# Performance work log

Hardware: AMD Instinct MI355X
Metric: run time of the kernel (lower is better)

The kernel has to match this reference:

```python
import jax, jax.numpy as jnp
import numpy as np

EPS = 1e-5
N_NODES = 100000
C_IN = 128
C_OUT = 128
N_EDGES = 3200000


def setup_inputs() -> dict:
    key = jax.random.key(0)
    k1, k2, k3 = jax.random.split(key, 3)
    x = jax.random.normal(k1, (N_NODES, C_IN), dtype=jnp.float32)
    edge_index = jax.random.randint(k2, (2, N_EDGES), 0, N_NODES, dtype=jnp.int64)
    # BatchNorm1d affine params
    gamma = jnp.ones((C_IN,), dtype=jnp.float32)
    beta = jnp.zeros((C_IN,), dtype=jnp.float32)
    # GCNConv linear weight (glorot) and bias
    limit = np.sqrt(6.0 / (C_IN + C_OUT)).astype(np.float32)
    W = jax.random.uniform(k3, (C_IN, C_OUT), minval=-limit, maxval=limit, dtype=jnp.float32)
    b = jnp.zeros((C_OUT,), dtype=jnp.float32)
    return {"x": x, "edge_index": edge_index, "gamma": gamma, "beta": beta, "W": W, "b": b}


def reference(x, edge_index, gamma, beta, W, b):
    n = x.shape[0]
    # --- BatchNorm1d (training mode: batch statistics, biased variance) ---
    mean = jnp.mean(x, axis=0)
    var = jnp.mean(jnp.square(x - mean), axis=0)
    xn = (x - mean) * jax.lax.rsqrt(var + EPS) * gamma + beta
    # --- GCNConv: linear, add self-loops, symmetric normalization, scatter-add ---
    h = xn @ W  # [n, C_out]
    loops = jnp.arange(n, dtype=edge_index.dtype)
    row = jnp.concatenate([edge_index[0], loops])  # source nodes
    col = jnp.concatenate([edge_index[1], loops])  # target nodes
    deg = jax.ops.segment_sum(jnp.ones_like(col, dtype=h.dtype), col, num_segments=n)
    dis = jnp.where(deg > 0, jax.lax.rsqrt(jnp.maximum(deg, 1.0)), 0.0)
    norm = dis[row] * dis[col]  # [E+n]
    msg = h[row] * norm[:, None]  # gather + scale
    out = jax.ops.segment_sum(msg, col, num_segments=n) + b  # scatter-add
    return jax.nn.relu(out)
```

## Files before the change

kernel.cpp:

```cpp
#include <hip/hip_runtime.h>

#define EPS_BN 1e-5f
#define C 128
#define CG 32
#define CAP 6144
#define NBLK 256

typedef __attribute__((ext_vector_type(8))) short bf16x8;
typedef __attribute__((ext_vector_type(4))) float f32x4;

__device__ inline unsigned bf16_rne(float f) {
  unsigned u = __float_as_uint(f);
  return (u + 0x7FFFu + ((u >> 16) & 1u)) >> 16;
}
__device__ inline float bf16_f(unsigned h) { return __uint_as_float(h << 16); }

__global__ void k_init(float* __restrict__ sums) {
  int i = blockIdx.x * blockDim.x + threadIdx.x;
  if (i < 256) sums[i] = 0.0f;
}

__global__ void k_stats(const float4* __restrict__ x4, float* __restrict__ sums, int n) {
  __shared__ float4 s_s[256];
  __shared__ float4 s_q[256];
  int t = threadIdx.x;
  int cg = t & 31;
  int rl = t >> 5;
  float4 s = make_float4(0.f, 0.f, 0.f, 0.f);
  float4 q = make_float4(0.f, 0.f, 0.f, 0.f);
  for (int r = blockIdx.x * 8 + rl; r < n; r += gridDim.x * 8) {
    float4 v = x4[(size_t)r * CG + cg];
    s.x += v.x; s.y += v.y; s.z += v.z; s.w += v.w;
    q.x += v.x * v.x; q.y += v.y * v.y; q.z += v.z * v.z; q.w += v.w * v.w;
  }
  s_s[t] = s; s_q[t] = q;
  __syncthreads();
  if (t < 32) {
    for (int j = 1; j < 8; ++j) {
      float4 a = s_s[t + 32 * j];
      float4 b = s_q[t + 32 * j];
      s.x += a.x; s.y += a.y; s.z += a.z; s.w += a.w;
      q.x += b.x; q.y += b.y; q.z += b.z; q.w += b.w;
    }
    atomicAdd(&sums[t * 4 + 0], s.x);
    atomicAdd(&sums[t * 4 + 1], s.y);
    atomicAdd(&sums[t * 4 + 2], s.z);
    atomicAdd(&sums[t * 4 + 3], s.w);
    atomicAdd(&sums[C + t * 4 + 0], q.x);
    atomicAdd(&sums[C + t * 4 + 1], q.y);
    atomicAdd(&sums[C + t * 4 + 2], q.z);
    atomicAdd(&sums[C + t * 4 + 3], q.w);
  }
}

__global__ void k_finalize(const float* __restrict__ sums,
                           const float* __restrict__ gamma,
                           const float* __restrict__ beta,
                           float* __restrict__ scale, float* __restrict__ shift,
                           int n) {
  int c = threadIdx.x;
  if (c < C) {
    float inv_n = 1.0f / (float)n;
    float mean = sums[c] * inv_n;
    float var = sums[C + c] * inv_n - mean * mean;
    float rstd = rsqrtf(var + EPS_BN);
    float sc = gamma[c] * rstd;
    scale[c] = sc;
    shift[c] = beta[c] - mean * sc;
  }
}

__global__ void k_hist(const int* __restrict__ col, int* __restrict__ histG,
                       int E, int NB, int chunk) {
  __shared__ int h[800];
  int b = blockIdx.x, t = threadIdx.x;
  for (int i = t; i < NB; i += 256) h[i] = 0;
  __syncthreads();
  int s = b * chunk, eend = min(E, s + chunk);
  for (int e = s + t; e < eend; e += 256) atomicAdd(&h[col[e] >> 7], 1);
  __syncthreads();
  for (int i = t; i < NB; i += 256) histG[b * NB + i] = h[i];
}

__global__ void k_scanH(int* __restrict__ histG, int* __restrict__ btot, int NB) {
  __shared__ int sh[NBLK];
  int q = blockIdx.x, t = threadIdx.x;
  int v = histG[t * NB + q];
  sh[t] = v;
  __syncthreads();
  for (int off = 1; off < NBLK; off <<= 1) {
    int a = (t >= off) ? sh[t - off] : 0;
    __syncthreads();
    sh[t] += a;
    __syncthreads();
  }
  histG[t * NB + q] = sh[t] - v;
  if (t == NBLK - 1) btot[q] = sh[t];
}

__global__ void k_scanB(const int* __restrict__ btot, int* __restrict__ boffs,
                        int NB, int E) {
  __shared__ int sh[1024];
  int t = threadIdx.x;
  int v = (t < NB) ? btot[t] : 0;
  sh[t] = v;
  __syncthreads();
  for (int off = 1; off < 1024; off <<= 1) {
    int a = (t >= off) ? sh[t - off] : 0;
    __syncthreads();
    sh[t] += a;
    __syncthreads();
  }
  if (t < NB) boffs[t] = sh[t] - v;
  if (t == 0) boffs[NB] = E;
}

__global__ void k_part(const int* __restrict__ row, const int* __restrict__ col,
                       const int* __restrict__ histG, const int* __restrict__ boffs,
                       unsigned* __restrict__ binned, int E, int NB, int chunk) {
  __shared__ int cur[800];
  int b = blockIdx.x, t = threadIdx.x;
  for (int i = t; i < NB; i += 256) cur[i] = boffs[i] + histG[b * NB + i];
  __syncthreads();
  int s = b * chunk, eend = min(E, s + chunk);
  for (int e = s + t; e < eend; e += 256) {
    int c = col[e];
    int pos = atomicAdd(&cur[c >> 7], 1);
    binned[pos] = ((unsigned)(c & 127) << 17) | (unsigned)row[e];
  }
}

__global__ __launch_bounds__(256) void k_reorder(
    unsigned* __restrict__ binned, const int* __restrict__ boffs,
    int* __restrict__ noffs, float* __restrict__ dis, int n, int E) {
  __shared__ int cnt[128];
  __shared__ int offs[128];
  __shared__ int cur[128];
  __shared__ int scn[128];
  __shared__ unsigned list[CAP];
  int b = blockIdx.x, t = threadIdx.x;
  if (t < 128) cnt[t] = 0;
  __syncthreads();
  int s = boffs[b], e = boffs[b + 1];
  for (int i = s + t; i < e; i += 256) atomicAdd(&cnt[binned[i] >> 17], 1);
  __syncthreads();
  if (t < 128) scn[t] = cnt[t];
  __syncthreads();
  for (int off = 1; off < 128; off <<= 1) {
    int a = (t >= off && t < 128) ? scn[t - off] : 0;
    __syncthreads();
    if (t < 128) scn[t] += a;
    __syncthreads();
  }
  if (t < 128) {
    offs[t] = scn[t] - cnt[t];
    cur[t] = scn[t] - cnt[t];
  }
  __syncthreads();
  for (int i = s + t; i < e; i += 256) {
    unsigned v = binned[i];
    int pos = atomicAdd(&cur[v >> 17], 1);
    if (pos < CAP) list[pos] = v & 0x1FFFFu;
  }
  __syncthreads();
  int len = e - s;
  for (int i = t; i < len; i += 256) binned[s + i] = list[i];
  int node = b * 128 + t;
  if (t < 128 && node < n) {
    noffs[node] = s + offs[t];
    dis[node] = rsqrtf((float)(cnt[t] + 1));
  }
  if (b == 0 && t == 0) noffs[n] = E;
}

__global__ void k_prep(const float2* __restrict__ x2, const float* __restrict__ dis,
                       const float2* __restrict__ scale2,
                       const float2* __restrict__ shift2,
                       unsigned* __restrict__ y, int n) {
  int idx = blockIdx.x * blockDim.x + threadIdx.x;
  int r = idx >> 6;
  if (r >= n) return;
  int lane = idx & 63;
  float d = dis[r];
  float2 v = x2[(size_t)r * 64 + lane];
  float2 sc = scale2[lane], sh = shift2[lane];
  float y0 = (v.x * sc.x + sh.x) * d;
  float y1 = (v.y * sc.y + sh.y) * d;
  y[(size_t)r * 64 + lane] = (bf16_rne(y1) << 16) | bf16_rne(y0);
}

__global__ __launch_bounds__(256) void k_G2(
    const unsigned* __restrict__ y, const unsigned* __restrict__ lst,
    const int* __restrict__ noffs, const float* __restrict__ dis,
    unsigned* __restrict__ ghi, unsigned* __restrict__ glo, int n) {
  int w = (blockIdx.x * blockDim.x + threadIdx.x) >> 6;
  if (w >= n) return;
  int lane = threadIdx.x & 63;
  int s = noffs[w], t = noffs[w + 1];
  float2 a0 = make_float2(0.f, 0.f), a1 = make_float2(0.f, 0.f);
  float2 a2 = make_float2(0.f, 0.f), a3 = make_float2(0.f, 0.f);
  int i = s;
  for (; i + 3 < t; i += 4) {
    int r0 = lst[i], r1 = lst[i + 1], r2 = lst[i + 2], r3 = lst[i + 3];
    unsigned u0 = y[(size_t)r0 * 64 + lane];
    unsigned u1 = y[(size_t)r1 * 64 + lane];
    unsigned u2 = y[(size_t)r2 * 64 + lane];
    unsigned u3 = y[(size_t)r3 * 64 + lane];
    a0.x += __uint_as_float(u0 << 16); a0.y += __uint_as_float(u0 & 0xFFFF0000u);
    a1.x += __uint_as_float(u1 << 16); a1.y += __uint_as_float(u1 & 0xFFFF0000u);
    a2.x += __uint_as_float(u2 << 16); a2.y += __uint_as_float(u2 & 0xFFFF0000u);
    a3.x += __uint_as_float(u3 << 16); a3.y += __uint_as_float(u3 & 0xFFFF0000u);
  }
  for (; i < t; ++i) {
    unsigned u = y[(size_t)lst[i] * 64 + lane];
    a0.x += __uint_as_float(u << 16); a0.y += __uint_as_float(u & 0xFFFF0000u);
  }
  unsigned uw = y[(size_t)w * 64 + lane];
  a0.x += __uint_as_float(uw << 16); a0.y += __uint_as_float(uw & 0xFFFF0000u);
  float dc = dis[w];
  float gx = dc * (a0.x + a1.x + a2.x + a3.x);
  float gy = dc * (a0.y + a1.y + a2.y + a3.y);
  unsigned hx = bf16_rne(gx), hy = bf16_rne(gy);
  unsigned lx = bf16_rne(gx - bf16_f(hx)), ly = bf16_rne(gy - bf16_f(hy));
  size_t o = (size_t)w * 64 + lane;
  ghi[o] = (hy << 16) | hx;
  glo[o] = (ly << 16) | lx;
}

__global__ __launch_bounds__(256) void k_gemmM(
    const unsigned* __restrict__ ghi, const unsigned* __restrict__ glo,
    const float* __restrict__ W, const float* __restrict__ bias,
    float* __restrict__ out, int n) {
  __shared__ __align__(16) unsigned short sGh[64][136];
  __shared__ __align__(16) unsigned short sGl[64][136];
  __shared__ __align__(16) unsigned short sWt[128][136];
  int t = threadIdx.x;
  int rowBase = blockIdx.x * 64;
  for (int i = t; i < 16384; i += 256) {
    int k = i >> 7, c = i & 127;
    sWt[c][k] = (unsigned short)bf16_rne(W[i]);
  }
  for (int i = t; i < 4096; i += 256) {
    int r = i >> 6, c = i & 63;
    int rw = rowBase + r;
    unsigned uh = 0, ul = 0;
    if (rw < n) {
      uh = ghi[(size_t)rw * 64 + c];
      ul = glo[(size_t)rw * 64 + c];
    }
    *(unsigned*)&sGh[r][c * 2] = uh;
    *(unsigned*)&sGl[r][c * 2] = ul;
  }
  __syncthreads();
  int w = t >> 6, l = t & 63;
  int m16 = l & 15, kb = l >> 4;
  int rtile = w * 16;
  f32x4 acc[8];
#pragma unroll
  for (int i = 0; i < 8; ++i) acc[i] = (f32x4){0.f, 0.f, 0.f, 0.f};
#pragma unroll
  for (int kt = 0; kt < 4; ++kt) {
    int koff = kt * 32 + kb * 8;
    bf16x8 ah = *(const bf16x8*)&sGh[rtile + m16][koff];
    bf16x8 al = *(const bf16x8*)&sGl[rtile + m16][koff];
#pragma unroll
    for (int nt = 0; nt < 8; ++nt) {
      bf16x8 bb = *(const bf16x8*)&sWt[nt * 16 + m16][koff];
      acc[nt] = __builtin_amdgcn_mfma_f32_16x16x32_bf16(ah, bb, acc[nt], 0, 0, 0);
      acc[nt] = __builtin_amdgcn_mfma_f32_16x16x32_bf16(al, bb, acc[nt], 0, 0, 0);
    }
  }
#pragma unroll
  for (int nt = 0; nt < 8; ++nt) {
    int colc = nt * 16 + m16;
    float bv = bias[colc];
#pragma unroll
    for (int reg = 0; reg < 4; ++reg) {
      int row = rowBase + rtile + kb * 4 + reg;
      if (row < n) {
        float o = acc[nt][reg] + bv;
        out[(size_t)row * C + colc] = fmaxf(o, 0.f);
      }
    }
  }
}

__global__ __launch_bounds__(256) void k_G(
    const unsigned* __restrict__ y, const unsigned* __restrict__ lst,
    const int* __restrict__ noffs, const float* __restrict__ dis,
    const float2* __restrict__ x2, const float2* __restrict__ scale2,
    const float2* __restrict__ shift2, float2* __restrict__ out2,
    int n, int useY) {
  int w = (blockIdx.x * blockDim.x + threadIdx.x) >> 6;
  if (w >= n) return;
  int lane = threadIdx.x & 63;
  int s = noffs[w], t = noffs[w + 1];
  float2 a0 = make_float2(0.f, 0.f), a1 = make_float2(0.f, 0.f);
  float2 a2 = make_float2(0.f, 0.f), a3 = make_float2(0.f, 0.f);
  if (useY) {
    int i = s;
    for (; i + 3 < t; i += 4) {
      int r0 = lst[i], r1 = lst[i + 1], r2 = lst[i + 2], r3 = lst[i + 3];
      unsigned u0 = y[(size_t)r0 * 64 + lane];
      unsigned u1 = y[(size_t)r1 * 64 + lane];
      unsigned u2 = y[(size_t)r2 * 64 + lane];
      unsigned u3 = y[(size_t)r3 * 64 + lane];
      a0.x += __uint_as_float(u0 << 16); a0.y += __uint_as_float(u0 & 0xFFFF0000u);
      a1.x += __uint_as_float(u1 << 16); a1.y += __uint_as_float(u1 & 0xFFFF0000u);
      a2.x += __uint_as_float(u2 << 16); a2.y += __uint_as_float(u2 & 0xFFFF0000u);
      a3.x += __uint_as_float(u3 << 16); a3.y += __uint_as_float(u3 & 0xFFFF0000u);
    }
    for (; i < t; ++i) {
      unsigned u = y[(size_t)lst[i] * 64 + lane];
      a0.x += __uint_as_float(u << 16); a0.y += __uint_as_float(u & 0xFFFF0000u);
    }
    float dc = dis[w];
    float2 o;
    o.x = dc * (a0.x + a1.x + a2.x + a3.x);
    o.y = dc * (a0.y + a1.y + a2.y + a3.y);
    out2[(size_t)w * 64 + lane] = o;
  } else {
    float sd = 0.f;
    for (int i = s; i < t; ++i) {
      int r = lst[i];
      float d = dis[r];
      float2 v = x2[(size_t)r * 64 + lane];
      a0.x += v.x * d; a0.y += v.y * d; sd += d;
    }
    float dc = dis[w];
    float2 sc = scale2[lane], sh = shift2[lane];
    float2 o;
    o.x = dc * (a0.x * sc.x + sd * sh.x);
    o.y = dc * (a0.y * sc.y + sd * sh.y);
    out2[(size_t)w * 64 + lane] = o;
  }
}

__global__ __launch_bounds__(256) void k_gemm(float* __restrict__ out,
                        const float4* __restrict__ x4,
                        const float* __restrict__ W,
                        const float* __restrict__ bias,
                        const float* __restrict__ scale,
                        const float* __restrict__ shift,
                        const float* __restrict__ dis, int n) {
  __shared__ float sW[64 * C];
  __shared__ float sG[32 * C];
  int t = threadIdx.x;
  int rowBase = blockIdx.x * 32;

  const float4* scale4 = (const float4*)scale;
  const float4* shift4 = (const float4*)shift;
  float4* sG4 = (float4*)sG;
  float4* sW4 = (float4*)sW;
  const float4* W4 = (const float4*)W;
  const float4* out4 = (const float4*)out;

  for (int i = t; i < 32 * CG; i += 256) {
    int r = i >> 5, g = i & 31;
    int rw = rowBase + r;
    float4 acc = make_float4(0.f, 0.f, 0.f, 0.f);
    if (rw < n) {
      acc = out4[(size_t)rw * CG + g];
      float4 xv = x4[(size_t)rw * CG + g];
      float d = dis[rw];
      float inv = d * d;
      float4 sc = scale4[g];
      float4 sh = shift4[g];
      acc.x += (xv.x * sc.x + sh.x) * inv;
      acc.y += (xv.y * sc.y + sh.y) * inv;
      acc.z += (xv.z * sc.z + sh.z) * inv;
      acc.w += (xv.w * sc.w + sh.w) * inv;
    }
    sG4[i] = acc;
  }

  int tx = t & 127;
  int ty = t >> 7;
  float acc[16];
#pragma unroll
  for (int i = 0; i < 16; ++i) acc[i] = 0.f;

  for (int kc = 0; kc < 2; ++kc) {
    for (int i = t; i < 64 * C / 4; i += 256) sW4[i] = W4[kc * 2048 + i];
    __syncthreads();
#pragma unroll 4
    for (int k = 0; k < 64; ++k) {
      float w = sW[k * C + tx];
#pragma unroll
      for (int rr = 0; rr < 16; ++rr)
        acc[rr] += sG[(rr * 2 + ty) * C + kc * 64 + k] * w;
    }
    __syncthreads();
  }

  float bv = bias[tx];
#pragma unroll
  for (int rr = 0; rr < 16; ++rr) {
    int rw = rowBase + rr * 2 + ty;
    if (rw < n) {
      float o = acc[rr] + bv;
      out[(size_t)rw * C + tx] = o > 0.f ? o : 0.f;
    }
  }
}

extern "C" void kernel_launch(void* const* d_in, const int* in_sizes, int n_in,
                              void* d_out, int out_size, void* d_ws, size_t ws_size,
                              hipStream_t stream) {
  const float* x = (const float*)d_in[0];
  const int* edge = (const int*)d_in[1];
  const float* gamma = (const float*)d_in[2];
  const float* beta = (const float*)d_in[3];
  const float* W = (const float*)d_in[4];
  const float* bias = (const float*)d_in[5];
  float* out = (float*)d_out;

  int n = in_sizes[0] / C;
  int E = in_sizes[1] / 2;
  int NB = (n + 127) / 128;
  int chunk = (E + NBLK - 1) / NBLK;

  float* ws = (float*)d_ws;
  float* sums = ws;
  float* scale = ws + 256;
  float* shift = ws + 384;
  float* dis = ws + 512;
  int* btot = (int*)(ws + 512 + n);
  int* boffs = btot + NB;
  int* noffs = boffs + NB + 1;
  int* histG = noffs + n + 1;
  unsigned* binned = (unsigned*)(histG + (size_t)NBLK * NB);
  unsigned* y = binned + E;
  unsigned* ghi = y + (size_t)n * 64;
  unsigned* glo = ghi + (size_t)n * 64;

  size_t base = (size_t)512 + n + NB + (NB + 1) + (n + 1) +
                (size_t)NBLK * NB + E;
  size_t need_old = base + (size_t)n * 64;
  size_t need_new = base + (size_t)n * 64 * 3;
  int mode = (ws_size >= need_new * 4) ? 2 : (ws_size >= need_old * 4) ? 1 : 0;

  k_init<<<1, 256, 0, stream>>>(sums);
  k_stats<<<256, 256, 0, stream>>>((const float4*)x, sums, n);
  k_finalize<<<1, 128, 0, stream>>>(sums, gamma, beta, scale, shift, n);
  k_hist<<<NBLK, 256, 0, stream>>>(edge + E, histG, E, NB, chunk);
  k_scanH<<<NB, NBLK, 0, stream>>>(histG, btot, NB);
  k_scanB<<<1, 1024, 0, stream>>>(btot, boffs, NB, E);
  k_part<<<NBLK, 256, 0, stream>>>(edge, edge + E, histG, boffs, binned, E, NB, chunk);
  k_reorder<<<NB, 256, 0, stream>>>(binned, boffs, noffs, dis, n, E);
  if (mode >= 1) {
    k_prep<<<(n * 64 + 255) / 256, 256, 0, stream>>>(
        (const float2*)x, dis, (const float2*)scale, (const float2*)shift, y, n);
  }
  if (mode == 2) {
    k_G2<<<(n * 64 + 255) / 256, 256, 0, stream>>>(y, binned, noffs, dis,
                                                   ghi, glo, n);
    k_gemmM<<<(n + 63) / 64, 256, 0, stream>>>(ghi, glo, W, bias, out, n);
  } else {
    k_G<<<(n * 64 + 255) / 256, 256, 0, stream>>>(
        y, binned, noffs, dis, (const float2*)x, (const float2*)scale,
        (const float2*)shift, (float2*)out, n, mode);
    k_gemm<<<(n + 31) / 32, 256, 0, stream>>>(out, (const float4*)x, W, bias,
                                              scale, shift, dis, n);
  }
}
```

Before: 349.0 us.

## Precompute bf16 transposed W, drop GEMM LDS staging, privatize reorder counters

Adds a one-off kernel that converts W to a transposed bf16 buffer, so the MFMA GEMM no longer converts and stages W into shared memory in every block. It also drops the staging of the ghi/glo tiles and loads MFMA operands straight from global memory. The reorder kernel now keeps per-wavefront counters to reduce shared-atomic contention. Hist and partition run with 512-thread blocks, stats uses more blocks, and a memset replaces the init kernel. Direct global loads in the GEMM may be less coalesced than the old shared-memory path.

Measured after the change: 391.8 us. 12.2% more time.

```diff
diff --git a/kernel.cpp b/kernel.cpp
--- a/kernel.cpp
+++ b/kernel.cpp
@@ -14,11 +14,6 @@
   return (u + 0x7FFFu + ((u >> 16) & 1u)) >> 16;
 }
 __device__ inline float bf16_f(unsigned h) { return __uint_as_float(h << 16); }
-
-__global__ void k_init(float* __restrict__ sums) {
-  int i = blockIdx.x * blockDim.x + threadIdx.x;
-  if (i < 256) sums[i] = 0.0f;
-}
 
 __global__ void k_stats(const float4* __restrict__ x4, float* __restrict__ sums, int n) {
   __shared__ float4 s_s[256];
@@ -70,16 +65,17 @@
   }
 }
 
-__global__ void k_hist(const int* __restrict__ col, int* __restrict__ histG,
-                       int E, int NB, int chunk) {
+__global__ __launch_bounds__(512) void k_hist(const int* __restrict__ col,
+                                              int* __restrict__ histG,
+                                              int E, int NB, int chunk) {
   __shared__ int h[800];
   int b = blockIdx.x, t = threadIdx.x;
-  for (int i = t; i < NB; i += 256) h[i] = 0;
+  for (int i = t; i < NB; i += 512) h[i] = 0;
   __syncthreads();
   int s = b * chunk, eend = min(E, s + chunk);
-  for (int e = s + t; e < eend; e += 256) atomicAdd(&h[col[e] >> 7], 1);
-  __syncthreads();
-  for (int i = t; i < NB; i += 256) histG[b * NB + i] = h[i];
+  for (int e = s + t; e < eend; e += 512) atomicAdd(&h[col[e] >> 7], 1);
+  __syncthreads();
+  for (int i = t; i < NB; i += 512) histG[b * NB + i] = h[i];
 }
 
 __global__ void k_scanH(int* __restrict__ histG, int* __restrict__ btot, int NB) {
@@ -115,15 +111,16 @@
   if (t == 0) boffs[NB] = E;
 }
 
-__global__ void k_part(const int* __restrict__ row, const int* __restrict__ col,
+__global__ __launch_bounds__(512) void k_part(const int* __restrict__ row,
+                       const int* __restrict__ col,
                        const int* __restrict__ histG, const int* __restrict__ boffs,
                        unsigned* __restrict__ binned, int E, int NB, int chunk) {
   __shared__ int cur[800];
   int b = blockIdx.x, t = threadIdx.x;
-  for (int i = t; i < NB; i += 256) cur[i] = boffs[i] + histG[b * NB + i];
+  for (int i = t; i < NB; i += 512) cur[i] = boffs[i] + histG[b * NB + i];
   __syncthreads();
   int s = b * chunk, eend = min(E, s + chunk);
-  for (int e = s + t; e < eend; e += 256) {
+  for (int e = s + t; e < eend; e += 512) {
     int c = col[e];
     int pos = atomicAdd(&cur[c >> 7], 1);
     binned[pos] = ((unsigned)(c & 127) << 17) | (unsigned)row[e];
@@ -133,18 +130,24 @@
 __global__ __launch_bounds__(256) void k_reorder(
     unsigned* __restrict__ binned, const int* __restrict__ boffs,
     int* __restrict__ noffs, float* __restrict__ dis, int n, int E) {
+  __shared__ int cnt4[4][128];
+  __shared__ int cur4[4][128];
   __shared__ int cnt[128];
   __shared__ int offs[128];
-  __shared__ int cur[128];
   __shared__ int scn[128];
   __shared__ unsigned list[CAP];
   int b = blockIdx.x, t = threadIdx.x;
-  if (t < 128) cnt[t] = 0;
+  int w = t >> 6;
+  for (int i = t; i < 512; i += 256) ((int*)cnt4)[i] = 0;
   __syncthreads();
   int s = boffs[b], e = boffs[b + 1];
-  for (int i = s + t; i < e; i += 256) atomicAdd(&cnt[binned[i] >> 17], 1);
-  __syncthreads();
-  if (t < 128) scn[t] = cnt[t];
+  for (int i = s + t; i < e; i += 256) atomicAdd(&cnt4[w][binned[i] >> 17], 1);
+  __syncthreads();
+  if (t < 128) {
+    int c0 = cnt4[0][t], c1 = cnt4[1][t], c2 = cnt4[2][t], c3 = cnt4[3][t];
+    cnt[t] = c0 + c1 + c2 + c3;
+    scn[t] = cnt[t];
+  }
   __syncthreads();
   for (int off = 1; off < 128; off <<= 1) {
     int a = (t >= off && t < 128) ? scn[t - off] : 0;
@@ -153,13 +156,17 @@
     __syncthreads();
   }
   if (t < 128) {
-    offs[t] = scn[t] - cnt[t];
-    cur[t] = scn[t] - cnt[t];
+    int o = scn[t] - cnt[t];
+    offs[t] = o;
+    cur4[0][t] = o;
+    cur4[1][t] = o + cnt4[0][t];
+    cur4[2][t] = o + cnt4[0][t] + cnt4[1][t];
+    cur4[3][t] = o + cnt4[0][t] + cnt4[1][t] + cnt4[2][t];
   }
   __syncthreads();
   for (int i = s + t; i < e; i += 256) {
     unsigned v = binned[i];
-    int pos = atomicAdd(&cur[v >> 17], 1);
+    int pos = atomicAdd(&cur4[w][v >> 17], 1);
     if (pos < CAP) list[pos] = v & 0x1FFFFu;
   }
   __syncthreads();
@@ -187,6 +194,14 @@
   float y0 = (v.x * sc.x + sh.x) * d;
   float y1 = (v.y * sc.y + sh.y) * d;
   y[(size_t)r * 64 + lane] = (bf16_rne(y1) << 16) | bf16_rne(y0);
+}
+
+__global__ void k_wt(const float* __restrict__ W, unsigned short* __restrict__ Wt) {
+  int i = blockIdx.x * 256 + threadIdx.x;
+  if (i < C * C) {
+    int k = i >> 7, c = i & 127;
+    Wt[c * C + k] = (unsigned short)bf16_rne(W[i]);
+  }
 }
 
 __global__ __launch_bounds__(256) void k_G2(
@@ -229,54 +244,39 @@
 
 __global__ __launch_bounds__(256) void k_gemmM(
     const unsigned* __restrict__ ghi, const unsigned* __restrict__ glo,
-    const float* __restrict__ W, const float* __restrict__ bias,
+    const unsigned short* __restrict__ Wt, const float* __restrict__ bias,
     float* __restrict__ out, int n) {
-  __shared__ __align__(16) unsigned short sGh[64][136];
-  __shared__ __align__(16) unsigned short sGl[64][136];
-  __shared__ __align__(16) unsigned short sWt[128][136];
   int t = threadIdx.x;
-  int rowBase = blockIdx.x * 64;
-  for (int i = t; i < 16384; i += 256) {
-    int k = i >> 7, c = i & 127;
-    sWt[c][k] = (unsigned short)bf16_rne(W[i]);
-  }
-  for (int i = t; i < 4096; i += 256) {
-    int r = i >> 6, c = i & 63;
-    int rw = rowBase + r;
-    unsigned uh = 0, ul = 0;
-    if (rw < n) {
-      uh = ghi[(size_t)rw * 64 + c];
-      ul = glo[(size_t)rw * 64 + c];
-    }
-    *(unsigned*)&sGh[r][c * 2] = uh;
-    *(unsigned*)&sGl[r][c * 2] = ul;
-  }
-  __syncthreads();
   int w = t >> 6, l = t & 63;
   int m16 = l & 15, kb = l >> 4;
-  int rtile = w * 16;
+  int rowA = blockIdx.x * 64 + w * 16 + m16;
+  int rowAc = min(rowA, n - 1);
+  const unsigned* gh = ghi + (size_t)rowAc * 64;
+  const unsigned* gl = glo + (size_t)rowAc * 64;
   f32x4 acc[8];
 #pragma unroll
   for (int i = 0; i < 8; ++i) acc[i] = (f32x4){0.f, 0.f, 0.f, 0.f};
 #pragma unroll
   for (int kt = 0; kt < 4; ++kt) {
+    int ko32 = kt * 16 + kb * 4;
     int koff = kt * 32 + kb * 8;
-    bf16x8 ah = *(const bf16x8*)&sGh[rtile + m16][koff];
-    bf16x8 al = *(const bf16x8*)&sGl[rtile + m16][koff];
+    bf16x8 ah = *(const bf16x8*)(gh + ko32);
+    bf16x8 al = *(const bf16x8*)(gl + ko32);
 #pragma unroll
     for (int nt = 0; nt < 8; ++nt) {
-      bf16x8 bb = *(const bf16x8*)&sWt[nt * 16 + m16][koff];
+      bf16x8 bb = *(const bf16x8*)(Wt + (nt * 16 + m16) * C + koff);
       acc[nt] = __builtin_amdgcn_mfma_f32_16x16x32_bf16(ah, bb, acc[nt], 0, 0, 0);
       acc[nt] = __builtin_amdgcn_mfma_f32_16x16x32_bf16(al, bb, acc[nt], 0, 0, 0);
     }
   }
+  int rowBase = blockIdx.x * 64 + w * 16;
 #pragma unroll
   for (int nt = 0; nt < 8; ++nt) {
     int colc = nt * 16 + m16;
     float bv = bias[colc];
 #pragma unroll
     for (int reg = 0; reg < 4; ++reg) {
-      int row = rowBase + rtile + kb * 4 + reg;
+      int row = rowBase + kb * 4 + reg;
       if (row < n) {
         float o = acc[nt][reg] + bv;
         out[(size_t)row * C + colc] = fmaxf(o, 0.f);
@@ -433,29 +433,32 @@
   unsigned* y = binned + E;
   unsigned* ghi = y + (size_t)n * 64;
   unsigned* glo = ghi + (size_t)n * 64;
+  unsigned short* Wt = (unsigned short*)(((uintptr_t)(glo + (size_t)n * 64) + 15) &
+                                         ~(uintptr_t)15);
 
   size_t base = (size_t)512 + n + NB + (NB + 1) + (n + 1) +
                 (size_t)NBLK * NB + E;
   size_t need_old = base + (size_t)n * 64;
-  size_t need_new = base + (size_t)n * 64 * 3;
+  size_t need_new = base + (size_t)n * 64 * 3 + 4096 + 8;
   int mode = (ws_size >= need_new * 4) ? 2 : (ws_size >= need_old * 4) ? 1 : 0;
 
-  k_init<<<1, 256, 0, stream>>>(sums);
-  k_stats<<<256, 256, 0, stream>>>((const float4*)x, sums, n);
+  hipMemsetAsync(sums, 0, 256 * sizeof(float), stream);
+  k_stats<<<1024, 256, 0, stream>>>((const float4*)x, sums, n);
   k_finalize<<<1, 128, 0, stream>>>(sums, gamma, beta, scale, shift, n);
-  k_hist<<<NBLK, 256, 0, stream>>>(edge + E, histG, E, NB, chunk);
+  k_hist<<<NBLK, 512, 0, stream>>>(edge + E, histG, E, NB, chunk);
   k_scanH<<<NB, NBLK, 0, stream>>>(histG, btot, NB);
   k_scanB<<<1, 1024, 0, stream>>>(btot, boffs, NB, E);
-  k_part<<<NBLK, 256, 0, stream>>>(edge, edge + E, histG, boffs, binned, E, NB, chunk);
+  k_part<<<NBLK, 512, 0, stream>>>(edge, edge + E, histG, boffs, binned, E, NB, chunk);
   k_reorder<<<NB, 256, 0, stream>>>(binned, boffs, noffs, dis, n, E);
   if (mode >= 1) {
     k_prep<<<(n * 64 + 255) / 256, 256, 0, stream>>>(
         (const float2*)x, dis, (const float2*)scale, (const float2*)shift, y, n);
   }
   if (mode == 2) {
+    k_wt<<<(C * C + 255) / 256, 256, 0, stream>>>(W, Wt);
     k_G2<<<(n * 64 + 255) / 256, 256, 0, stream>>>(y, binned, noffs, dis,
                                                    ghi, glo, n);
-    k_gemmM<<<(n + 63) / 64, 256, 0, stream>>>(ghi, glo, W, bias, out, n);
+    k_gemmM<<<(n + 63) / 64, 256, 0, stream>>>(ghi, glo, Wt, bias, out, n);
   } else {
     k_G<<<(n * 64 + 255) / 256, 256, 0, stream>>>(
         y, binned, noffs, dis, (const float2*)x, (const float2*)scale,
```
